# Optimization experiments

Measured on AMD Instinct MI355X. Metric: run time of the kernel, lower is better.

Reference implementation:

```python
import jax, jax.numpy as jnp
import numpy as np
from jax import lax

IN_C, OUT_C = 256, 128
HID = (IN_C // 8) // 2   # hidden_channels = 16
NL = 9                   # num_layer
SHIFTS = (1, 5)
DN = ('NCHW', 'OIHW', 'NCHW')

def _base_kernels():
    d1 = np.zeros((4, 1, 3, 3), np.float32)
    d1[0, 0, 0, 0] = -1.0
    d1[1, 0, 0, 1] = -1.0
    d1[2, 0, 0, 2] = -1.0
    d1[3, 0, 1, 2] = -1.0
    d2 = d1[:, :, ::-1, ::-1].copy()
    return np.concatenate([d1, d2], 0)  # (8,1,3,3)

# each of the 8 fixed shift kernels tiled per channel -> (8, HID, 1, 3, 3)
_KER = jnp.asarray(np.tile(_base_kernels()[:, None], (1, HID, 1, 1, 1)))

def _branch(cen, in_w, in_b, w1, w2, w3, sc, shift):
    # input projection conv (kernel 1 or 3, 'same' padding)
    h = lax.conv_general_dilated(cen, in_w, (1, 1), 'SAME', dimension_numbers=DN)
    h = h + in_b[None, :, None, None]
    # 8 fixed dilated depthwise 3x3 convs
    deltas = [lax.conv_general_dilated(h, _KER[k], (1, 1), 'SAME',
                                       rhs_dilation=(shift, shift),
                                       feature_group_count=HID,
                                       dimension_numbers=DN)
              for k in range(8)]
    x = jnp.concatenate(deltas + [h], 1)  # (b, NL*HID, H, W)
    b, c, H, W = x.shape
    xg = x.reshape(b, NL, HID, H, W)
    # grouped 1x1 convs (groups=NL) == per-group 16x16 matmuls
    o1 = jnp.einsum('gdc,bgchw->bgdhw', w1, xg)
    o2 = jnp.einsum('gdc,bgchw->bgdhw', w2, xg)
    o3 = jnp.einsum('gdc,bgchw->bgdhw', w3, xg)
    # logits[b,p,q,h,w] = sc * sum_c o2[b,p,c]*o1[b,q,c]  (torch sums dim=3 of out1*out2*scale)
    logits = sc * jnp.einsum('bpchw,bqchw->bpqhw', o2, o1)
    attn = jax.nn.softmax(logits, axis=2)  # softmax over q (torch dim=2)
    out = jnp.einsum('bpqhw,bqchw->bpchw', attn, o3)
    return out.reshape(b, NL * HID, H, W)

def setup_inputs():
    key = jax.random.key(0)
    ks = jax.random.split(key, 16)
    B, H, W = 4, 192, 192
    s = 0.05
    return {
        'cen': jax.random.normal(ks[0], (B, IN_C, H, W), jnp.float32),
        'in_w0': jax.random.normal(ks[1], (HID, IN_C, 1, 1), jnp.float32) * s,
        'in_b0': jax.random.normal(ks[2], (HID,), jnp.float32) * s,
        'in_w1': jax.random.normal(ks[3], (HID, IN_C, 3, 3), jnp.float32) * s,
        'in_b1': jax.random.normal(ks[4], (HID,), jnp.float32) * s,
        'w1_0': jax.random.normal(ks[5], (NL, HID, HID), jnp.float32) * s,
        'w2_0': jax.random.normal(ks[6], (NL, HID, HID), jnp.float32) * s,
        'w3_0': jax.random.normal(ks[7], (NL, HID, HID), jnp.float32) * s,
        'w1_1': jax.random.normal(ks[8], (NL, HID, HID), jnp.float32) * s,
        'w2_1': jax.random.normal(ks[9], (NL, HID, HID), jnp.float32) * s,
        'w3_1': jax.random.normal(ks[10], (NL, HID, HID), jnp.float32) * s,
        'scale': jax.random.normal(ks[11], (len(SHIFTS),), jnp.float32) * s,
        'out_w': jax.random.normal(ks[12], (OUT_C, NL * HID * len(SHIFTS), 1, 1), jnp.float32) * s,
        'out_b': jax.random.normal(ks[13], (OUT_C,), jnp.float32) * s,
    }

def reference(cen, in_w0, in_b0, in_w1, in_b1, w1_0, w2_0, w3_0,
              w1_1, w2_1, w3_1, scale, out_w, out_b):
    o0 = _branch(cen, in_w0, in_b0, w1_0, w2_0, w3_0, scale[0], SHIFTS[0])
    o1 = _branch(cen, in_w1, in_b1, w1_1, w2_1, w3_1, scale[1], SHIFTS[1])
    cat = jnp.concatenate([o0, o1], 1)  # (b, 288, H, W)
    return jnp.einsum('oi,bihw->bohw', out_w[:, :, 0, 0], cat) + out_b[None, :, None, None]
```

## Files before the change

kernel.cpp:

```cpp
#include <hip/hip_runtime.h>
#include <hip/hip_bf16.h>
#include <cstddef>
#include <cstdint>

#define BATCH 4
#define INC   256
#define HID   16
#define NL    9
#define HH    192
#define WW    192
#define PIX   (HH*WW)
#define BPIX  (BATCH*PIX)
#define OUTC  128
#define CATC  (NL*HID*2)
#define CATK  160

#define KCSTRIDE (WW*32)
#define ROWSTRIDE (8*WW*32)

typedef __attribute__((ext_vector_type(8))) short bf16x8;
typedef __attribute__((ext_vector_type(4))) float f32x4;
typedef unsigned short ushort_t;

__device__ inline unsigned short f2bf(float f) {
  unsigned int u = __float_as_uint(f);
  u += 0x7FFF + ((u >> 16) & 1);
  return (unsigned short)(u >> 16);
}
__device__ inline float bf2f(unsigned short s) {
  return __uint_as_float(((unsigned)s) << 16);
}
__device__ inline unsigned pack2(float a, float b) {
  return (unsigned)f2bf(a) | ((unsigned)f2bf(b) << 16);
}
__device__ inline bf16x8 cvt8(float4 a, float4 b) {
  union { bf16x8 v; unsigned u[4]; } r;
  r.u[0] = pack2(a.x, a.y); r.u[1] = pack2(a.z, a.w);
  r.u[2] = pack2(b.x, b.y); r.u[3] = pack2(b.z, b.w);
  return r.v;
}

__global__ __launch_bounds__(256) void kernelP(const float* __restrict__ cen,
                                               ushort_t* __restrict__ th,
                                               ushort_t* __restrict__ tl) {
  __shared__ float t[256][17];
  const int b = blockIdx.z, y = blockIdx.y, x0 = blockIdx.x * 16;
  const int tid = threadIdx.x;
#pragma unroll
  for (int k = 0; k < 16; ++k) {
    int i = tid + k * 256; int c = i >> 4, xl = i & 15;
    t[c][xl] = cen[((size_t)(b * 256 + c)) * PIX + (size_t)y * WW + x0 + xl];
  }
  __syncthreads();
  const size_t rowbase = (size_t)(b * HH + y) * ROWSTRIDE;
  const int kcq = tid >> 5;
  const int c32 = tid & 31;
  const size_t obase = rowbase + (size_t)kcq * KCSTRIDE + c32;
#pragma unroll
  for (int xl = 0; xl < 16; ++xl) {
    float v = t[tid][xl];
    unsigned short hi = f2bf(v);
    const size_t a = obase + (size_t)(x0 + xl) * 32;
    th[a] = hi;
    tl[a] = f2bf(v - bf2f(hi));
  }
}

__global__ __launch_bounds__(256) void wprepA(
    const float* __restrict__ w0, const float* __restrict__ w1,
    ushort_t* __restrict__ wA0hi, ushort_t* __restrict__ wA0lo,
    ushort_t* __restrict__ wA1hi, ushort_t* __restrict__ wA1lo) {
  int idx = blockIdx.x * 256 + threadIdx.x;
  if (idx < 36864) {
    int j = idx & 7, l = (idx >> 3) & 63, kc = (idx >> 9) & 7, s = idx >> 12;
    int d = l & 15, c = kc * 32 + (l >> 4) * 8 + j;
    float v = w1[(size_t)(d * 256 + c) * 9 + s];
    unsigned short hi = f2bf(v);
    wA1hi[idx] = hi; wA1lo[idx] = f2bf(v - bf2f(hi));
  }
  if (idx < 4096) {
    int j = idx & 7, l = (idx >> 3) & 63, kc = idx >> 9;
    int d = l & 15, c = kc * 32 + (l >> 4) * 8 + j;
    float v = w0[d * 256 + c];
    unsigned short hi = f2bf(v);
    wA0hi[idx] = hi; wA0lo[idx] = f2bf(v - bf2f(hi));
  }
}

__global__ __launch_bounds__(256) void wprepB(const float* __restrict__ out_w,
                                              ushort_t* __restrict__ wb) {
  int idx = blockIdx.x * 256 + threadIdx.x;
  if (idx >= 2 * OUTC * CATK) return;
  int k = idx % CATK; int rest = idx / CATK;
  int o = rest % OUTC; int br = rest / OUTC;
  float v = (k < 144) ? out_w[o * CATC + br * 144 + k] : 0.f;
  wb[idx] = f2bf(v);
}

__global__ __launch_bounds__(256) void wprepM(
    const float* __restrict__ w1_0, const float* __restrict__ w2_0,
    const float* __restrict__ w3_0, const float* __restrict__ w1_1,
    const float* __restrict__ w2_1, const float* __restrict__ w3_1,
    ushort_t* __restrict__ wm) {
  int idx = blockIdx.x * 256 + threadIdx.x;
  if (idx >= 2 * 27 * 512) return;
  int j = idx & 7;
  int lane = (idx >> 3) & 63;
  int blk = idx >> 9;
  int g = blk % 9, mat = (blk / 9) % 3, br = blk / 27;
  int d = lane & 15, k = (lane >> 4) * 8 + j;
  float v = 0.f;
  if (k < 16) {
    const float* w;
    if (br == 0) w = (mat == 0) ? w1_0 : (mat == 1) ? w2_0 : w3_0;
    else         w = (mat == 0) ? w1_1 : (mat == 1) ? w2_1 : w3_1;
    v = w[(g * 16 + d) * 16 + k];
    if (g < 8) v = -v;
  }
  wm[idx] = f2bf(v);
}

template <bool SAFE>
__device__ inline void a_tile(const ushort_t* __restrict__ th,
                              const ushort_t* __restrict__ tl,
                              const ushort_t* __restrict__ wA0hi,
                              const ushort_t* __restrict__ wA0lo,
                              const ushort_t* __restrict__ wA1hi,
                              const ushort_t* __restrict__ wA1lo,
                              int b, int y, int px, f32x4& acc0, f32x4& acc1) {
  const int lane = threadIdx.x & 63;
  const int quad = lane >> 4;
  const bf16x8 bz = {0, 0, 0, 0, 0, 0, 0, 0};
#pragma unroll
  for (int sy = 0; sy < 3; ++sy) {
    const int yy = y + sy - 1;
    const bool yok = SAFE || ((unsigned)yy < (unsigned)HH);
#pragma unroll
    for (int sx = 0; sx < 3; ++sx) {
      const int xx = px + sx - 1;
      const bool ok = SAFE || (yok && ((unsigned)xx < (unsigned)WW));
      const int cy = SAFE ? yy : (ok ? yy : 0);
      const int cx = SAFE ? xx : (ok ? xx : 0);
      const size_t base =
          (size_t)(b * HH + cy) * ROWSTRIDE + (size_t)cx * 32 + quad * 8;
      const int s = sy * 3 + sx;
      const ushort_t* wh = wA1hi + s * 4096 + lane * 8;
      const ushort_t* wl = wA1lo + s * 4096 + lane * 8;

      bf16x8 bh[8], bl[8];
#pragma unroll
      for (int kc = 0; kc < 8; ++kc) {
        bh[kc] = *(const bf16x8*)(th + base + kc * KCSTRIDE);
        bl[kc] = *(const bf16x8*)(tl + base + kc * KCSTRIDE);
      }
      if (!SAFE && !ok) {
#pragma unroll
        for (int kc = 0; kc < 8; ++kc) { bh[kc] = bz; bl[kc] = bz; }
      }

#pragma unroll
      for (int kc = 0; kc < 8; ++kc) {
        bf16x8 ahi = *(const bf16x8*)(wh + kc * 512);
        bf16x8 alo = *(const bf16x8*)(wl + kc * 512);
        acc1 = __builtin_amdgcn_mfma_f32_16x16x32_bf16(ahi, bh[kc], acc1, 0, 0, 0);
        acc1 = __builtin_amdgcn_mfma_f32_16x16x32_bf16(ahi, bl[kc], acc1, 0, 0, 0);
        acc1 = __builtin_amdgcn_mfma_f32_16x16x32_bf16(alo, bh[kc], acc1, 0, 0, 0);
        if (s == 4) {
          bf16x8 a0h = *(const bf16x8*)(wA0hi + kc * 512 + lane * 8);
          bf16x8 a0l = *(const bf16x8*)(wA0lo + kc * 512 + lane * 8);
          acc0 = __builtin_amdgcn_mfma_f32_16x16x32_bf16(a0h, bh[kc], acc0, 0, 0, 0);
          acc0 = __builtin_amdgcn_mfma_f32_16x16x32_bf16(a0h, bl[kc], acc0, 0, 0, 0);
          acc0 = __builtin_amdgcn_mfma_f32_16x16x32_bf16(a0l, bh[kc], acc0, 0, 0, 0);
        }
      }
    }
  }
}

__global__ __launch_bounds__(256) void kernelA_mfma(
    const ushort_t* __restrict__ th, const ushort_t* __restrict__ tl,
    const ushort_t* __restrict__ wA0hi, const ushort_t* __restrict__ wA0lo,
    const ushort_t* __restrict__ wA1hi, const ushort_t* __restrict__ wA1lo,
    const float* __restrict__ b0, const float* __restrict__ b1,
    float* __restrict__ h0, float* __restrict__ h1) {
  const int lt = blockIdx.x;
  const int xb = lt % 3;
  const int y  = (lt / 3) % HH;
  const int b  = lt / (3 * HH);

  const int lane = threadIdx.x & 63, wave = threadIdx.x >> 6;
  const int n = lane & 15, quad = lane >> 4;
  const int wpx0 = xb * 64 + wave * 16;
  const int px = wpx0 + n;
  f32x4 acc0 = {0.f, 0.f, 0.f, 0.f}, acc1 = {0.f, 0.f, 0.f, 0.f};

  const bool safe = (y >= 1) && (y <= HH - 2) && (wpx0 >= 1) && (wpx0 + 16 <= WW - 1);
  if (safe)
    a_tile<true>(th, tl, wA0hi, wA0lo, wA1hi, wA1lo, b, y, px, acc0, acc1);
  else
    a_tile<false>(th, tl, wA0hi, wA0lo, wA1hi, wA1lo, b, y, px, acc0, acc1);

  const size_t pb = ((size_t)b * PIX + (size_t)y * WW + px) * 16 + quad * 4;
  float4 r0, r1;
  r0.x = acc0[0] + b0[quad * 4 + 0]; r0.y = acc0[1] + b0[quad * 4 + 1];
  r0.z = acc0[2] + b0[quad * 4 + 2]; r0.w = acc0[3] + b0[quad * 4 + 3];
  r1.x = acc1[0] + b1[quad * 4 + 0]; r1.y = acc1[1] + b1[quad * 4 + 1];
  r1.z = acc1[2] + b1[quad * 4 + 2]; r1.w = acc1[3] + b1[quad * 4 + 3];
  *(float4*)(h0 + pb) = r0;
  *(float4*)(h1 + pb) = r1;
}

__global__ __launch_bounds__(256) void kernelA_f32(
    const float* __restrict__ cen, const float* __restrict__ w0,
    const float* __restrict__ b0,  const float* __restrict__ w1,
    const float* __restrict__ b1,  float* __restrict__ h0,
    float* __restrict__ h1) {
  __shared__ float lds[16 * 18 * 18];
  const int lx = threadIdx.x, ly = threadIdx.y;
  const int tid = ly * 16 + lx;
  const int x0 = blockIdx.x * 16, y0 = blockIdx.y * 16, b = blockIdx.z;

  float acc0[16], acc1[16];
#pragma unroll
  for (int d = 0; d < 16; ++d) { acc0[d] = 0.f; acc1[d] = 0.f; }

  for (int cb = 0; cb < INC; cb += 16) {
    __syncthreads();
    for (int i = tid; i < 16 * 18 * 18; i += 256) {
      int c = i / 324; int rem = i - c * 324;
      int yy = rem / 18; int xx = rem - yy * 18;
      int gy = y0 + yy - 1, gx = x0 + xx - 1;
      float v = 0.f;
      if (gy >= 0 && gy < HH && gx >= 0 && gx < WW)
        v = cen[(((size_t)b * INC + cb + c) * HH + gy) * WW + gx];
      lds[i] = v;
    }
    __syncthreads();
    for (int c = 0; c < 16; ++c) {
      float v[9];
#pragma unroll
      for (int r = 0; r < 9; ++r) {
        const int dy = r / 3, dx = r - (r / 3) * 3;
        v[r] = lds[(c * 18 + ly + dy) * 18 + lx + dx];
      }
      const int cc = cb + c;
#pragma unroll
      for (int d = 0; d < 16; ++d)
        acc0[d] = fmaf(w0[d * INC + cc], v[4], acc0[d]);
#pragma unroll
      for (int d = 0; d < 16; ++d) {
        float a = acc1[d];
#pragma unroll
        for (int r = 0; r < 9; ++r)
          a = fmaf(w1[(d * INC + cc) * 9 + r], v[r], a);
        acc1[d] = a;
      }
    }
  }
  const int y = y0 + ly, x = x0 + lx;
  const size_t base = ((size_t)b * PIX + (size_t)y * WW + x) * 16;
#pragma unroll
  for (int k = 0; k < 4; ++k) {
    float4 r0, r1;
    r0.x = acc0[4 * k + 0] + b0[4 * k + 0]; r0.y = acc0[4 * k + 1] + b0[4 * k + 1];
    r0.z = acc0[4 * k + 2] + b0[4 * k + 2]; r0.w = acc0[4 * k + 3] + b0[4 * k + 3];
    r1.x = acc1[4 * k + 0] + b1[4 * k + 0]; r1.y = acc1[4 * k + 1] + b1[4 * k + 1];
    r1.z = acc1[4 * k + 2] + b1[4 * k + 2]; r1.w = acc1[4 * k + 3] + b1[4 * k + 3];
    *(float4*)(h0 + base + 4 * k) = r0;
    *(float4*)(h1 + base + 4 * k) = r1;
  }
}

template <int SHIFT, int BRANCH>
__global__ __launch_bounds__(256) void kernelB1m(
    const float* __restrict__ h,
    const ushort_t* __restrict__ wm,
    const float* __restrict__ scale, ushort_t* __restrict__ cat) {
  const int lane = threadIdx.x & 63;
  const int gw = blockIdx.x * 4 + (threadIdx.x >> 6);
  const int bpix0 = gw * 16;
  const int b = bpix0 / PIX;
  const int rem = bpix0 - b * PIX;
  const int y = rem / WW, x0 = rem - y * WW;
  const int n = lane & 15, quad = lane >> 4;
  const float sc = scale[BRANCH];
  const float* __restrict__ hb = h + (size_t)b * PIX * 16;
  const ushort_t* __restrict__ wmb = wm + (size_t)BRANCH * 27 * 512;

  constexpr int DY[9] = {-1, -1, -1, 0, 1, 1, 1, 0, 0};
  constexpr int DX[9] = {-1, 0, 1, 1, 1, 0, -1, -1, 0};

  bf16x8 xf[9];
#pragma unroll
  for (int g = 0; g < 9; ++g) {
    bf16x8 v = {0, 0, 0, 0, 0, 0, 0, 0};
    const int yy = y + DY[g] * SHIFT;
    const int xx = x0 + n + DX[g] * SHIFT;
    if (quad < 2 && (unsigned)yy < (unsigned)HH && (unsigned)xx < (unsigned)WW) {
      const float4* p = (const float4*)(hb + ((size_t)yy * WW + xx) * 16 + quad * 8);
      v = cvt8(p[0], p[1]);
    }
    xf[g] = v;
  }

  const f32x4 zero4 = {0.f, 0.f, 0.f, 0.f};
  f32x4 o1[9], o3[9];
#pragma unroll
  for (int g = 0; g < 9; ++g) {
    const bf16x8 a1 = *(const bf16x8*)(wmb + (0 * 9 + g) * 512 + lane * 8);
    o1[g] = __builtin_amdgcn_mfma_f32_16x16x32_bf16(a1, xf[g], zero4, 0, 0, 0);
  }
#pragma unroll
  for (int g = 0; g < 9; ++g) {
    const bf16x8 a3 = *(const bf16x8*)(wmb + (2 * 9 + g) * 512 + lane * 8);
    o3[g] = __builtin_amdgcn_mfma_f32_16x16x32_bf16(a3, xf[g], zero4, 0, 0, 0);
  }

  ushort_t* __restrict__ crow = cat + (size_t)(bpix0 + n) * CATK;

#pragma unroll
  for (int p = 0; p < 9; ++p) {
    const bf16x8 a2 = *(const bf16x8*)(wmb + (1 * 9 + p) * 512 + lane * 8);
    const f32x4 o2p = __builtin_amdgcn_mfma_f32_16x16x32_bf16(a2, xf[p], zero4, 0, 0, 0);
    float e[9]; float m = -1e30f;
#pragma unroll
    for (int q = 0; q < 9; ++q) {
      float t = (o2p[0] * o1[q][0] + o2p[1] * o1[q][1]) +
                (o2p[2] * o1[q][2] + o2p[3] * o1[q][3]);
      t += __shfl_xor(t, 16);
      t += __shfl_xor(t, 32);
      e[q] = sc * t;
      m = fmaxf(m, e[q]);
    }
    float s = 0.f;
#pragma unroll
    for (int q = 0; q < 9; ++q) { e[q] = __expf(e[q] - m); s += e[q]; }
    const float inv = 1.0f / s;
    f32x4 ov = zero4;
#pragma unroll
    for (int q = 0; q < 9; ++q) {
      const float a = e[q] * inv;
      ov[0] = fmaf(a, o3[q][0], ov[0]);
      ov[1] = fmaf(a, o3[q][1], ov[1]);
      ov[2] = fmaf(a, o3[q][2], ov[2]);
      ov[3] = fmaf(a, o3[q][3], ov[3]);
    }
    uint2 w; w.x = pack2(ov[0], ov[1]); w.y = pack2(ov[2], ov[3]);
    *(uint2*)(crow + p * 16 + quad * 4) = w;
  }
  if (quad < 2)
    *(uint4*)(crow + 144 + quad * 8) = make_uint4(0, 0, 0, 0);
}

template <int BRANCH, bool ACCUM>
__global__ __launch_bounds__(256) void kernelB2(
    const ushort_t* __restrict__ cat, const ushort_t* __restrict__ wb,
    const float* __restrict__ out_b, float* __restrict__ out) {
  const int wave = threadIdx.x >> 6;
  const int lane = threadIdx.x & 63;
  const int tile = blockIdx.x * 4 + wave;
  const int bpix0 = tile * 16;
  const int n = lane & 15, quad = lane >> 4;

  const bf16x8* __restrict__ bp =
      (const bf16x8*)(cat + (size_t)(bpix0 + n) * CATK + quad * 8);
  const ushort_t* __restrict__ wrow0 =
      wb + ((size_t)BRANCH * OUTC + n) * CATK + quad * 8;

  f32x4 acc[8];
#pragma unroll
  for (int mt = 0; mt < 8; ++mt) acc[mt] = (f32x4){0.f, 0.f, 0.f, 0.f};

#pragma unroll
  for (int kc = 0; kc < 5; ++kc) {
    const bf16x8 bfrag = bp[kc * 4];
#pragma unroll
    for (int mt = 0; mt < 8; ++mt) {
      const bf16x8 afrag =
          *(const bf16x8*)(wrow0 + (size_t)mt * 16 * CATK + kc * 32);
      acc[mt] = __builtin_amdgcn_mfma_f32_16x16x32_bf16(afrag, bfrag, acc[mt], 0, 0, 0);
    }
  }

  const int b = bpix0 / PIX;
  const int pin = bpix0 - b * PIX + n;
#pragma unroll
  for (int mt = 0; mt < 8; ++mt) {
#pragma unroll
    for (int i = 0; i < 4; ++i) {
      const int o = mt * 16 + quad * 4 + i;
      const size_t addr = ((size_t)(b * OUTC + o)) * PIX + pin;
      float r = acc[mt][i];
      if (ACCUM) r += out[addr]; else r += out_b[o];
      out[addr] = r;
    }
  }
}

__global__ __launch_bounds__(256) void kernelB2fused(
    const ushort_t* __restrict__ cat0, const ushort_t* __restrict__ cat1,
    const ushort_t* __restrict__ wb, const float* __restrict__ out_b,
    float* __restrict__ out) {
  const int wave = threadIdx.x >> 6;
  const int lane = threadIdx.x & 63;
  const int tile = blockIdx.x * 4 + wave;
  const int bpix0 = tile * 16;
  const int n = lane & 15, quad = lane >> 4;

  f32x4 acc[8];
#pragma unroll
  for (int mt = 0; mt < 8; ++mt) acc[mt] = (f32x4){0.f, 0.f, 0.f, 0.f};

#pragma unroll
  for (int br = 0; br < 2; ++br) {
    const ushort_t* cp = br ? cat1 : cat0;
    const bf16x8* __restrict__ bp =
        (const bf16x8*)(cp + (size_t)(bpix0 + n) * CATK + quad * 8);
    const ushort_t* __restrict__ wrow0 =
        wb + ((size_t)br * OUTC + n) * CATK + quad * 8;
#pragma unroll
    for (int kc = 0; kc < 5; ++kc) {
      const bf16x8 bfrag = bp[kc * 4];
#pragma unroll
      for (int mt = 0; mt < 8; ++mt) {
        const bf16x8 afrag =
            *(const bf16x8*)(wrow0 + (size_t)mt * 16 * CATK + kc * 32);
        acc[mt] = __builtin_amdgcn_mfma_f32_16x16x32_bf16(afrag, bfrag, acc[mt], 0, 0, 0);
      }
    }
  }

  const int b = bpix0 / PIX;
  const int pin = bpix0 - b * PIX + n;
#pragma unroll
  for (int mt = 0; mt < 8; ++mt) {
#pragma unroll
    for (int i = 0; i < 4; ++i) {
      const int o = mt * 16 + quad * 4 + i;
      const size_t addr = ((size_t)(b * OUTC + o)) * PIX + pin;
      out[addr] = acc[mt][i] + out_b[o];
    }
  }
}

extern "C" void kernel_launch(void* const* d_in, const int* in_sizes, int n_in,
                              void* d_out, int out_size, void* d_ws, size_t ws_size,
                              hipStream_t stream) {
  const float* cen   = (const float*)d_in[0];
  const float* in_w0 = (const float*)d_in[1];
  const float* in_b0 = (const float*)d_in[2];
  const float* in_w1 = (const float*)d_in[3];
  const float* in_b1 = (const float*)d_in[4];
  const float* w1_0  = (const float*)d_in[5];
  const float* w2_0  = (const float*)d_in[6];
  const float* w3_0  = (const float*)d_in[7];
  const float* w1_1  = (const float*)d_in[8];
  const float* w2_1  = (const float*)d_in[9];
  const float* w3_1  = (const float*)d_in[10];
  const float* scale = (const float*)d_in[11];
  const float* out_w = (const float*)d_in[12];
  const float* out_b = (const float*)d_in[13];
  float* out = (float*)d_out;

  const size_t H_ELEMS = (size_t)BATCH * HID * PIX;
  const size_t PLANE_E = (size_t)BPIX * 256;
  const size_t CAT_E   = (size_t)BPIX * CATK;

  float* h0 = (float*)d_ws;
  float* h1 = h0 + H_ELEMS;
  ushort_t* wsm = (ushort_t*)(h1 + H_ELEMS);
  ushort_t* wA0hi = wsm;
  ushort_t* wA0lo = wsm + 4096;
  ushort_t* wA1hi = wsm + 8192;
  ushort_t* wA1lo = wsm + 45056;
  ushort_t* wb    = wsm + 81920;
  ushort_t* wm    = wsm + 122880;
  ushort_t* big   = wsm + 150528;

  const size_t base_bytes = 2 * H_ELEMS * 4 + 150528 * 2;
  const size_t fast_need       = base_bytes + 2 * PLANE_E * 2;
  const size_t slow_fused_need = base_bytes + 2 * CAT_E * 2;
  const bool fast  = ws_size >= fast_need;
  const bool fused = fast || ws_size >= slow_fused_need;

  ushort_t* cat0 = big;
  ushort_t* cat1 = fused ? (big + CAT_E) : big;

  hipLaunchKernelGGL(wprepB, dim3((2 * OUTC * CATK + 255) / 256), dim3(256), 0,
                     stream, out_w, wb);
  hipLaunchKernelGGL(wprepM, dim3((2 * 27 * 512 + 255) / 256), dim3(256), 0,
                     stream, w1_0, w2_0, w3_0, w1_1, w2_1, w3_1, wm);

  if (fast) {
    ushort_t* th = big;
    ushort_t* tl = big + PLANE_E;
    hipLaunchKernelGGL(wprepA, dim3(144), dim3(256), 0, stream,
                       in_w0, in_w1, wA0hi, wA0lo, wA1hi, wA1lo);
    hipLaunchKernelGGL(kernelP, dim3(WW / 16, HH, BATCH), dim3(256), 0, stream,
                       cen, th, tl);
    hipLaunchKernelGGL(kernelA_mfma, dim3(3 * HH * BATCH), dim3(256), 0, stream,
                       th, tl, wA0hi, wA0lo, wA1hi, wA1lo, in_b0, in_b1, h0, h1);
  } else {
    hipLaunchKernelGGL(kernelA_f32, dim3(WW / 16, HH / 16, BATCH), dim3(16, 16), 0,
                       stream, cen, in_w0, in_b0, in_w1, in_b1, h0, h1);
  }

  const int nb1 = (BPIX / 16) / 4;
  const int nb2 = (BPIX / 16) / 4;

  if (fused) {
    hipLaunchKernelGGL((kernelB1m<1, 0>), dim3(nb1), dim3(256), 0, stream,
                       h0, wm, scale, cat0);
    hipLaunchKernelGGL((kernelB1m<5, 1>), dim3(nb1), dim3(256), 0, stream,
                       h1, wm, scale, cat1);
    hipLaunchKernelGGL(kernelB2fused, dim3(nb2), dim3(256), 0, stream,
                       cat0, cat1, wb, out_b, out);
  } else {
    hipLaunchKernelGGL((kernelB1m<1, 0>), dim3(nb1), dim3(256), 0, stream,
                       h0, wm, scale, cat0);
    hipLaunchKernelGGL((kernelB2<0, false>), dim3(nb2), dim3(256), 0, stream,
                       cat0, wb, out_b, out);
    hipLaunchKernelGGL((kernelB1m<5, 1>), dim3(nb1), dim3(256), 0, stream,
                       h1, w1_1 ? wm : wm, scale, cat1);
    hipLaunchKernelGGL((kernelB2<1, true>), dim3(nb2), dim3(256), 0, stream,
                       cat1, wb, out_b, out);
  }
}
```

Measured before the change: 642.8 us.

## Tile kernelA over four output rows to reuse loaded input rows across taps

```diff
diff --git a/kernel.cpp b/kernel.cpp
--- a/kernel.cpp
+++ b/kernel.cpp
@@ -14,6 +14,7 @@
 #define OUTC  128
 #define CATC  (NL*HID*2)
 #define CATK  160
+#define BY    4
 
 #define KCSTRIDE (WW*32)
 #define ROWSTRIDE (8*WW*32)
@@ -120,64 +121,87 @@
   wm[idx] = f2bf(v);
 }
 
-template <bool SAFE>
-__device__ inline void a_tile(const ushort_t* __restrict__ th,
+template <bool SAFEX, bool SAFEY>
+__device__ inline void a_rows(const ushort_t* __restrict__ th,
                               const ushort_t* __restrict__ tl,
                               const ushort_t* __restrict__ wA0hi,
                               const ushort_t* __restrict__ wA0lo,
                               const ushort_t* __restrict__ wA1hi,
                               const ushort_t* __restrict__ wA1lo,
-                              int b, int y, int px, f32x4& acc0, f32x4& acc1) {
+                              int b, int y0, int px,
+                              f32x4 (&acc0)[BY], f32x4 (&acc1)[BY]) {
   const int lane = threadIdx.x & 63;
   const int quad = lane >> 4;
   const bf16x8 bz = {0, 0, 0, 0, 0, 0, 0, 0};
-#pragma unroll
-  for (int sy = 0; sy < 3; ++sy) {
-    const int yy = y + sy - 1;
-    const bool yok = SAFE || ((unsigned)yy < (unsigned)HH);
-#pragma unroll
-    for (int sx = 0; sx < 3; ++sx) {
-      const int xx = px + sx - 1;
-      const bool ok = SAFE || (yok && ((unsigned)xx < (unsigned)WW));
-      const int cy = SAFE ? yy : (ok ? yy : 0);
-      const int cx = SAFE ? xx : (ok ? xx : 0);
-      const size_t base =
-          (size_t)(b * HH + cy) * ROWSTRIDE + (size_t)cx * 32 + quad * 8;
-      const int s = sy * 3 + sx;
-      const ushort_t* wh = wA1hi + s * 4096 + lane * 8;
-      const ushort_t* wl = wA1lo + s * 4096 + lane * 8;
-
-      bf16x8 bh[8], bl[8];
-#pragma unroll
-      for (int kc = 0; kc < 8; ++kc) {
-        bh[kc] = *(const bf16x8*)(th + base + kc * KCSTRIDE);
-        bl[kc] = *(const bf16x8*)(tl + base + kc * KCSTRIDE);
-      }
-      if (!SAFE && !ok) {
-#pragma unroll
-        for (int kc = 0; kc < 8; ++kc) { bh[kc] = bz; bl[kc] = bz; }
-      }
-
-#pragma unroll
-      for (int kc = 0; kc < 8; ++kc) {
-        bf16x8 ahi = *(const bf16x8*)(wh + kc * 512);
-        bf16x8 alo = *(const bf16x8*)(wl + kc * 512);
-        acc1 = __builtin_amdgcn_mfma_f32_16x16x32_bf16(ahi, bh[kc], acc1, 0, 0, 0);
-        acc1 = __builtin_amdgcn_mfma_f32_16x16x32_bf16(ahi, bl[kc], acc1, 0, 0, 0);
-        acc1 = __builtin_amdgcn_mfma_f32_16x16x32_bf16(alo, bh[kc], acc1, 0, 0, 0);
-        if (s == 4) {
-          bf16x8 a0h = *(const bf16x8*)(wA0hi + kc * 512 + lane * 8);
-          bf16x8 a0l = *(const bf16x8*)(wA0lo + kc * 512 + lane * 8);
-          acc0 = __builtin_amdgcn_mfma_f32_16x16x32_bf16(a0h, bh[kc], acc0, 0, 0, 0);
-          acc0 = __builtin_amdgcn_mfma_f32_16x16x32_bf16(a0h, bl[kc], acc0, 0, 0, 0);
-          acc0 = __builtin_amdgcn_mfma_f32_16x16x32_bf16(a0l, bh[kc], acc0, 0, 0, 0);
+
+  int cxs[3]; bool okx[3];
+#pragma unroll
+  for (int sx = 0; sx < 3; ++sx) {
+    const int xx = px + sx - 1;
+    okx[sx] = SAFEX || ((unsigned)xx < (unsigned)WW);
+    cxs[sx] = okx[sx] ? xx : 0;
+  }
+
+#pragma unroll
+  for (int ri = 0; ri <= BY + 1; ++ri) {
+    const int r = y0 - 1 + ri;
+    if (!SAFEY && ((unsigned)r >= (unsigned)HH)) continue;
+    const size_t rowb = (size_t)(b * HH + r) * ROWSTRIDE + quad * 8;
+#pragma unroll
+    for (int kc4 = 0; kc4 < 8; kc4 += 4) {
+      bf16x8 dh[3][4], dl[3][4];
+#pragma unroll
+      for (int sx = 0; sx < 3; ++sx) {
+        const size_t base = rowb + (size_t)cxs[sx] * 32 + (size_t)kc4 * KCSTRIDE;
+#pragma unroll
+        for (int k = 0; k < 4; ++k) {
+          dh[sx][k] = *(const bf16x8*)(th + base + k * KCSTRIDE);
+          dl[sx][k] = *(const bf16x8*)(tl + base + k * KCSTRIDE);
         }
       }
-    }
-  }
-}
-
-__global__ __launch_bounds__(256) void kernelA_mfma(
+      if (!SAFEX) {
+#pragma unroll
+        for (int sx = 0; sx < 3; ++sx) {
+          if (!okx[sx]) {
+#pragma unroll
+            for (int k = 0; k < 4; ++k) { dh[sx][k] = bz; dl[sx][k] = bz; }
+          }
+        }
+      }
+#pragma unroll
+      for (int sy = 0; sy < 3; ++sy) {
+        const int oi = ri - sy;
+        if (oi < 0 || oi >= BY) continue;
+#pragma unroll
+        for (int sx = 0; sx < 3; ++sx) {
+          const int s = sy * 3 + sx;
+          const ushort_t* wh = wA1hi + s * 4096 + kc4 * 512 + lane * 8;
+          const ushort_t* wl = wA1lo + s * 4096 + kc4 * 512 + lane * 8;
+#pragma unroll
+          for (int k = 0; k < 4; ++k) {
+            const bf16x8 ahi = *(const bf16x8*)(wh + k * 512);
+            const bf16x8 alo = *(const bf16x8*)(wl + k * 512);
+            acc1[oi] = __builtin_amdgcn_mfma_f32_16x16x32_bf16(ahi, dh[sx][k], acc1[oi], 0, 0, 0);
+            acc1[oi] = __builtin_amdgcn_mfma_f32_16x16x32_bf16(ahi, dl[sx][k], acc1[oi], 0, 0, 0);
+            acc1[oi] = __builtin_amdgcn_mfma_f32_16x16x32_bf16(alo, dh[sx][k], acc1[oi], 0, 0, 0);
+          }
+        }
+        if (sy == 1) {
+#pragma unroll
+          for (int k = 0; k < 4; ++k) {
+            const bf16x8 a0h = *(const bf16x8*)(wA0hi + (kc4 + k) * 512 + lane * 8);
+            const bf16x8 a0l = *(const bf16x8*)(wA0lo + (kc4 + k) * 512 + lane * 8);
+            acc0[oi] = __builtin_amdgcn_mfma_f32_16x16x32_bf16(a0h, dh[1][k], acc0[oi], 0, 0, 0);
+            acc0[oi] = __builtin_amdgcn_mfma_f32_16x16x32_bf16(a0h, dl[1][k], acc0[oi], 0, 0, 0);
+            acc0[oi] = __builtin_amdgcn_mfma_f32_16x16x32_bf16(a0l, dh[1][k], acc0[oi], 0, 0, 0);
+          }
+        }
+      }
+    }
+  }
+}
+
+__global__ __launch_bounds__(256, 2) void kernelA_mfma(
     const ushort_t* __restrict__ th, const ushort_t* __restrict__ tl,
     const ushort_t* __restrict__ wA0hi, const ushort_t* __restrict__ wA0lo,
     const ushort_t* __restrict__ wA1hi, const ushort_t* __restrict__ wA1lo,
@@ -185,29 +209,50 @@
     float* __restrict__ h0, float* __restrict__ h1) {
   const int lt = blockIdx.x;
   const int xb = lt % 3;
-  const int y  = (lt / 3) % HH;
-  const int b  = lt / (3 * HH);
+  const int by = (lt / 3) % (HH / BY);
+  const int b  = lt / (3 * (HH / BY));
+  const int y0 = by * BY;
 
   const int lane = threadIdx.x & 63, wave = threadIdx.x >> 6;
   const int n = lane & 15, quad = lane >> 4;
   const int wpx0 = xb * 64 + wave * 16;
   const int px = wpx0 + n;
-  f32x4 acc0 = {0.f, 0.f, 0.f, 0.f}, acc1 = {0.f, 0.f, 0.f, 0.f};
-
-  const bool safe = (y >= 1) && (y <= HH - 2) && (wpx0 >= 1) && (wpx0 + 16 <= WW - 1);
-  if (safe)
-    a_tile<true>(th, tl, wA0hi, wA0lo, wA1hi, wA1lo, b, y, px, acc0, acc1);
-  else
-    a_tile<false>(th, tl, wA0hi, wA0lo, wA1hi, wA1lo, b, y, px, acc0, acc1);
-
-  const size_t pb = ((size_t)b * PIX + (size_t)y * WW + px) * 16 + quad * 4;
-  float4 r0, r1;
-  r0.x = acc0[0] + b0[quad * 4 + 0]; r0.y = acc0[1] + b0[quad * 4 + 1];
-  r0.z = acc0[2] + b0[quad * 4 + 2]; r0.w = acc0[3] + b0[quad * 4 + 3];
-  r1.x = acc1[0] + b1[quad * 4 + 0]; r1.y = acc1[1] + b1[quad * 4 + 1];
-  r1.z = acc1[2] + b1[quad * 4 + 2]; r1.w = acc1[3] + b1[quad * 4 + 3];
-  *(float4*)(h0 + pb) = r0;
-  *(float4*)(h1 + pb) = r1;
+
+  f32x4 acc0[BY], acc1[BY];
+#pragma unroll
+  for (int oi = 0; oi < BY; ++oi) {
+    acc0[oi] = (f32x4){0.f, 0.f, 0.f, 0.f};
+    acc1[oi] = (f32x4){0.f, 0.f, 0.f, 0.f};
+  }
+
+  const bool safex = (wpx0 >= 1) && (wpx0 + 16 <= WW - 1);
+  const bool safey = (y0 >= 1) && (y0 + BY <= HH - 1);
+  if (safex) {
+    if (safey) a_rows<true, true >(th, tl, wA0hi, wA0lo, wA1hi, wA1lo, b, y0, px, acc0, acc1);
+    else       a_rows<true, false>(th, tl, wA0hi, wA0lo, wA1hi, wA1lo, b, y0, px, acc0, acc1);
+  } else {
+    if (safey) a_rows<false, true >(th, tl, wA0hi, wA0lo, wA1hi, wA1lo, b, y0, px, acc0, acc1);
+    else       a_rows<false, false>(th, tl, wA0hi, wA0lo, wA1hi, wA1lo, b, y0, px, acc0, acc1);
+  }
+
+  float bias0[4], bias1[4];
+#pragma unroll
+  for (int i = 0; i < 4; ++i) {
+    bias0[i] = b0[quad * 4 + i];
+    bias1[i] = b1[quad * 4 + i];
+  }
+#pragma unroll
+  for (int oi = 0; oi < BY; ++oi) {
+    const int y = y0 + oi;
+    const size_t pb = ((size_t)b * PIX + (size_t)y * WW + px) * 16 + quad * 4;
+    float4 r0, r1;
+    r0.x = acc0[oi][0] + bias0[0]; r0.y = acc0[oi][1] + bias0[1];
+    r0.z = acc0[oi][2] + bias0[2]; r0.w = acc0[oi][3] + bias0[3];
+    r1.x = acc1[oi][0] + bias1[0]; r1.y = acc1[oi][1] + bias1[1];
+    r1.z = acc1[oi][2] + bias1[2]; r1.w = acc1[oi][3] + bias1[3];
+    *(float4*)(h0 + pb) = r0;
+    *(float4*)(h1 + pb) = r1;
+  }
 }
 
 __global__ __launch_bounds__(256) void kernelA_f32(
@@ -498,8 +543,9 @@
                        in_w0, in_w1, wA0hi, wA0lo, wA1hi, wA1lo);
     hipLaunchKernelGGL(kernelP, dim3(WW / 16, HH, BATCH), dim3(256), 0, stream,
                        cen, th, tl);
-    hipLaunchKernelGGL(kernelA_mfma, dim3(3 * HH * BATCH), dim3(256), 0, stream,
-                       th, tl, wA0hi, wA0lo, wA1hi, wA1lo, in_b0, in_b1, h0, h1);
+    hipLaunchKernelGGL(kernelA_mfma, dim3(3 * (HH / BY) * BATCH), dim3(256), 0,
+                       stream, th, tl, wA0hi, wA0lo, wA1hi, wA1lo, in_b0, in_b1,
+                       h0, h1);
   } else {
     hipLaunchKernelGGL(kernelA_f32, dim3(WW / 16, HH / 16, BATCH), dim3(16, 16), 0,
                        stream, cen, in_w0, in_b0, in_w1, in_b1, h0, h1);
```

Result: slower. 976.9 us (+52.0%).
